# Kernel tuning notes

Measured on AMD Instinct MI355X. Metric: run time of the kernel, lower is better.

Reference implementation:

```python
import jax, jax.numpy as jnp
import numpy as np


def setup_inputs() -> dict:
    key = jax.random.key(0)
    B, N = 32, 2048
    x = jax.random.normal(key, (B, N), dtype=jnp.float32)
    return {"input": x}


def reference(input) -> jnp.ndarray:
    # pair[b, i, j] = sigmoid(input[b, j] - input[b, i])  -> [B, N, N]
    pair = jax.nn.sigmoid(input[:, None, :] - input[:, :, None])
    # rr[b, i] = 1 / (sum_j pair[b, i, j] + 0.5)          -> [B, N]
    rr = 1.0 / (jnp.sum(pair, axis=-1) + 0.5)
    # loss uses only row 0 (positive doc's soft reciprocal rank)
    loss = -jnp.mean(rr[:, 0])
    return loss
```

## Files before the change

kernel.cpp:

```cpp
#include <hip/hip_runtime.h>


#define RL_B 32
#define RL_N 2048

__device__ __forceinline__ float sig(float d) {
    return 1.0f / (1.0f + __expf(-d));
}

__global__ __launch_bounds__(64) void RankLoss_73959336837390_rows(
    const float* __restrict__ x, float* __restrict__ partial) {
    const int b    = blockIdx.x;
    const int lane = threadIdx.x;

    const float* __restrict__ row = x + b * RL_N;
    const float4* __restrict__ r4 = (const float4*)row;

    const float x0 = row[0];

    float4 v[8];
    #pragma unroll
    for (int k = 0; k < 8; ++k) v[k] = r4[lane + (k << 6)];

    float s = 0.0f;
    #pragma unroll
    for (int k = 0; k < 8; ++k) {
        s += sig(v[k].x - x0) + sig(v[k].y - x0)
           + sig(v[k].z - x0) + sig(v[k].w - x0);
    }

    #pragma unroll
    for (int off = 32; off > 0; off >>= 1) s += __shfl_xor(s, off, 64);

    if (lane == 0) partial[b] = 1.0f / (s + 0.5f);
}

__global__ __launch_bounds__(64) void RankLoss_73959336837390_reduce(
    const float* __restrict__ partial, float* __restrict__ out) {
    const int lane = threadIdx.x;
    float v = (lane < RL_B) ? partial[lane] : 0.0f;
    #pragma unroll
    for (int off = 32; off > 0; off >>= 1) v += __shfl_xor(v, off, 64);
    if (lane == 0) *out = -v / (float)RL_B;
}

extern "C" void kernel_launch(void* const* d_in, const int* in_sizes, int n_in,
                              void* d_out, int out_size, void* d_ws, size_t ws_size,
                              hipStream_t stream) {
    const float* x = (const float*)d_in[0];
    float* out     = (float*)d_out;
    float* partial = (float*)d_ws;

    RankLoss_73959336837390_rows<<<RL_B, 64, 0, stream>>>(x, partial);
    RankLoss_73959336837390_reduce<<<1, 64, 0, stream>>>(partial, out);
}
```

Baseline: 55.29 us.

## Fuse row and reduce kernels via cooperative grid sync, widen blocks to 256 threads

Merges the per-row kernel and the final reduction kernel into one cooperative launch that uses a grid-wide sync before block 0 sums the per-row partials. Each block now has 256 threads (4 waves) doing two float4 loads each instead of one wave doing eight, combined through shared memory. The aim is to remove a second kernel launch and shorten each block's serial work. The cost is the overhead of a cooperative launch and the grid barrier, which can exceed a plain launch for such a tiny workload.

```diff
diff --git a/kernel.cpp b/kernel.cpp
--- a/kernel.cpp
+++ b/kernel.cpp
@@ -1,4 +1,7 @@
 #include <hip/hip_runtime.h>
+#include <hip/hip_cooperative_groups.h>
+
+namespace cg = cooperative_groups;
 
 
 #define RL_B 32
@@ -8,40 +11,46 @@
     return 1.0f / (1.0f + __expf(-d));
 }
 
-__global__ __launch_bounds__(64) void RankLoss_73959336837390_rows(
-    const float* __restrict__ x, float* __restrict__ partial) {
+__global__ __launch_bounds__(256) void RankLoss_73959336837390_fused(
+    const float* __restrict__ x, float* __restrict__ partial,
+    float* __restrict__ out) {
     const int b    = blockIdx.x;
-    const int lane = threadIdx.x;
+    const int tid  = threadIdx.x;
+    const int wave = tid >> 6;
+    const int lane = tid & 63;
+
+    __shared__ float ws[4];
 
     const float* __restrict__ row = x + b * RL_N;
     const float4* __restrict__ r4 = (const float4*)row;
 
     const float x0 = row[0];
 
-    float4 v[8];
-    #pragma unroll
-    for (int k = 0; k < 8; ++k) v[k] = r4[lane + (k << 6)];
+    float4 v0 = r4[tid];
+    float4 v1 = r4[tid + 256];
 
-    float s = 0.0f;
-    #pragma unroll
-    for (int k = 0; k < 8; ++k) {
-        s += sig(v[k].x - x0) + sig(v[k].y - x0)
-           + sig(v[k].z - x0) + sig(v[k].w - x0);
-    }
+    float s = sig(v0.x - x0) + sig(v0.y - x0) + sig(v0.z - x0) + sig(v0.w - x0)
+            + sig(v1.x - x0) + sig(v1.y - x0) + sig(v1.z - x0) + sig(v1.w - x0);
 
     #pragma unroll
     for (int off = 32; off > 0; off >>= 1) s += __shfl_xor(s, off, 64);
+    if (lane == 0) ws[wave] = s;
+    __syncthreads();
 
-    if (lane == 0) partial[b] = 1.0f / (s + 0.5f);
-}
+    if (tid == 0) {
+        float t = ws[0] + ws[1] + ws[2] + ws[3];
+        partial[b] = 1.0f / (t + 0.5f);
+    }
+    __threadfence();
 
-__global__ __launch_bounds__(64) void RankLoss_73959336837390_reduce(
-    const float* __restrict__ partial, float* __restrict__ out) {
-    const int lane = threadIdx.x;
-    float v = (lane < RL_B) ? partial[lane] : 0.0f;
-    #pragma unroll
-    for (int off = 32; off > 0; off >>= 1) v += __shfl_xor(v, off, 64);
-    if (lane == 0) *out = -v / (float)RL_B;
+    cg::this_grid().sync();
+
+    if (b == 0 && wave == 0) {
+        float v = (lane < RL_B) ? partial[lane] : 0.0f;
+        #pragma unroll
+        for (int off = 32; off > 0; off >>= 1) v += __shfl_xor(v, off, 64);
+        if (lane == 0) *out = -v / (float)RL_B;
+    }
 }
 
 extern "C" void kernel_launch(void* const* d_in, const int* in_sizes, int n_in,
@@ -51,6 +60,7 @@
     float* out     = (float*)d_out;
     float* partial = (float*)d_ws;
 
-    RankLoss_73959336837390_rows<<<RL_B, 64, 0, stream>>>(x, partial);
-    RankLoss_73959336837390_reduce<<<1, 64, 0, stream>>>(partial, out);
+    void* args[] = {(void*)&x, (void*)&partial, (void*)&out};
+    hipLaunchCooperativeKernel((const void*)RankLoss_73959336837390_fused,
+                               dim3(RL_B), dim3(256), args, 0, stream);
 }
```

Measured after the change: 79.87 us. +44.5%, slower.
